# Kernel optimization log

Measured on AMD Instinct MI355X. Metric: run time of the kernel, lower is better.

Reference implementation:

```python
import jax, jax.numpy as jnp
import numpy as np

L, H, E, T, B, V = 8, 16, 1024, 1024, 2, 800
D = E // H  # head_size = 64
STD = 0.02


def setup_inputs() -> dict:
    key = jax.random.key(0)
    ks = iter(jax.random.split(key, 32))

    def nrm(shape):
        return jax.random.normal(next(ks), shape, jnp.float32) * STD

    latlong = jax.random.uniform(next(ks), (B, T, 2), jnp.float32)
    wl = jax.random.uniform(next(ks), (B, T, 1), jnp.float32, minval=3.0, maxval=11.0)
    inp = {
        "idx": jnp.concatenate([latlong, wl], axis=-1),  # [B,T,3]
        "tok_table": nrm((V, E)),
        "pos_W": nrm((2, E)),
        "pos_b": jnp.zeros((E,), jnp.float32),
        # stacked per-layer params (per-head q/k/v linears fused into [E,E])
        "Wq": nrm((L, E, E)),
        "Wk": nrm((L, E, E)),
        "Wv": nrm((L, E, E)),
        "Wo": nrm((L, E, E)),
        "bo": jnp.zeros((L, E), jnp.float32),
        "W1": nrm((L, E, 4 * E)),
        "b1": jnp.zeros((L, 4 * E), jnp.float32),
        "W2": nrm((L, 4 * E, E)),
        "b2": jnp.zeros((L, E), jnp.float32),
        "ln1_g": jnp.ones((L, E), jnp.float32),
        "ln1_b": jnp.zeros((L, E), jnp.float32),
        "ln2_g": jnp.ones((L, E), jnp.float32),
        "ln2_b": jnp.zeros((L, E), jnp.float32),
        "lnf_g": jnp.ones((E,), jnp.float32),
        "lnf_b": jnp.zeros((E,), jnp.float32),
        "lm_W": nrm((E, V)),
        "lm_b": jnp.zeros((V,), jnp.float32),
    }
    return inp


def _ln(x, g, b, eps=1e-5):
    m = x.mean(-1, keepdims=True)
    v = x.var(-1, keepdims=True)
    return (x - m) * jax.lax.rsqrt(v + eps) * g + b


def _block(x, p):
    Wq, Wk, Wv, Wo, bo, W1, b1, W2, b2, g1, be1, g2, be2 = p
    Bx, Tx, _ = x.shape
    h = _ln(x, g1, be1)
    q = (h @ Wq).reshape(Bx, Tx, H, D)
    k = (h @ Wk).reshape(Bx, Tx, H, D)
    v = (h @ Wv).reshape(Bx, Tx, H, D)
    scores = jnp.einsum('bqhd,bkhd->bhqk', q, k) * (D ** -0.5)
    mask = jnp.tril(jnp.ones((Tx, Tx), bool))  # causal
    scores = jnp.where(mask, scores, -jnp.inf)
    w = jax.nn.softmax(scores, axis=-1)  # dropout=0 (eval) -> identity
    attn = jnp.einsum('bhqk,bkhd->bqhd', w, v).reshape(Bx, Tx, E)
    x = x + attn @ Wo + bo
    h = _ln(x, g2, be2)
    x = x + jax.nn.relu(h @ W1 + b1) @ W2 + b2
    return x


def reference(idx, tok_table, pos_W, pos_b, Wq, Wk, Wv, Wo, bo, W1, b1, W2, b2,
              ln1_g, ln1_b, ln2_g, ln2_b, lnf_g, lnf_b, lm_W, lm_b):
    # water level channel -> token id in [0, V-1]
    idx_wl = jnp.clip(jnp.round(idx[..., 2] * 100.0 - 300.0), 0, V - 1).astype(jnp.int32)
    tok_emb = tok_table[idx_wl]                      # [B,T,E]
    pos_emb = idx[..., :2] @ pos_W + pos_b           # [B,T,E]
    x = tok_emb + pos_emb

    params = (Wq, Wk, Wv, Wo, bo, W1, b1, W2, b2, ln1_g, ln1_b, ln2_g, ln2_b)

    def body(carry, p):
        return _block(carry, p), None

    x, _ = jax.lax.scan(body, x, params)
    x = _ln(x, lnf_g, lnf_b)
    logits = x @ lm_W + lm_b                         # [B,T,V]
    return logits
```

## Files before the change

### kernel.cpp

```cpp
#include <hip/hip_runtime.h>
#include <hip/hip_bf16.h>

#define L_ 8
#define H_ 16
#define E_ 1024
#define T_ 1024
#define B_ 2
#define V_ 800
#define D_ 64
#define FF_ 4096
#define N_ (B_ * T_)
#define QS_ 3072

typedef unsigned short u16;
typedef __bf16 bf16x8 __attribute__((ext_vector_type(8)));
typedef float f32x4 __attribute__((ext_vector_type(4)));

__device__ __forceinline__ u16 f2b(float f) {
    unsigned int u = __float_as_uint(f);
    unsigned int r = (u + 0x7fffu + ((u >> 16) & 1u)) >> 16;
    return (u16)r;
}

__device__ __forceinline__ void gld16(const u16* g, u16* l) {
    __builtin_amdgcn_global_load_lds(
        (__attribute__((address_space(1))) void*)(uintptr_t)g,
        (__attribute__((address_space(3))) void*)(unsigned)(uintptr_t)l,
        16, 0, 0);
}

__global__ __launch_bounds__(256) void embed_ln_k(
    const float* __restrict__ idx, const float* __restrict__ tok,
    const float* __restrict__ posW, const float* __restrict__ posb,
    const float* __restrict__ g, const float* __restrict__ bta,
    float* __restrict__ x, u16* __restrict__ out)
{
    __shared__ float rs[4], rq[4];
    int row = blockIdx.x;
    int tid = threadIdx.x;
    int e = tid * 4;
    float lat = idx[row * 3 + 0];
    float lon = idx[row * 3 + 1];
    float wl  = idx[row * 3 + 2];
    float tf = rintf(wl * 100.0f - 300.0f);
    tf = fminf(fmaxf(tf, 0.0f), (float)(V_ - 1));
    int tkn = (int)tf;

    float4 tv = *(const float4*)(tok + (size_t)tkn * E_ + e);
    float4 p0 = *(const float4*)(posW + e);
    float4 p1 = *(const float4*)(posW + E_ + e);
    float4 pb = *(const float4*)(posb + e);
    float4 xv;
    xv.x = tv.x + lat * p0.x + lon * p1.x + pb.x;
    xv.y = tv.y + lat * p0.y + lon * p1.y + pb.y;
    xv.z = tv.z + lat * p0.z + lon * p1.z + pb.z;
    xv.w = tv.w + lat * p0.w + lon * p1.w + pb.w;
    *(float4*)(x + (size_t)row * E_ + e) = xv;

    float s = xv.x + xv.y + xv.z + xv.w;
    float q = xv.x * xv.x + xv.y * xv.y + xv.z * xv.z + xv.w * xv.w;
    #pragma unroll
    for (int off = 32; off; off >>= 1) {
        s += __shfl_xor(s, off, 64);
        q += __shfl_xor(q, off, 64);
    }
    int wv = tid >> 6, ln = tid & 63;
    if (ln == 0) { rs[wv] = s; rq[wv] = q; }
    __syncthreads();
    s = rs[0] + rs[1] + rs[2] + rs[3];
    q = rq[0] + rq[1] + rq[2] + rq[3];
    float mean = s * (1.0f / E_);
    float var  = q * (1.0f / E_) - mean * mean;
    float inv  = 1.0f / sqrtf(var + 1e-5f);
    float4 gv = *(const float4*)(g + e);
    float4 bv = *(const float4*)(bta + e);
    ushort4 ov;
    ov.x = f2b((xv.x - mean) * inv * gv.x + bv.x);
    ov.y = f2b((xv.y - mean) * inv * gv.y + bv.y);
    ov.z = f2b((xv.z - mean) * inv * gv.z + bv.z);
    ov.w = f2b((xv.w - mean) * inv * gv.w + bv.w);
    *(ushort4*)(out + (size_t)row * E_ + e) = ov;
}

__global__ __launch_bounds__(256) void ln_k(
    const float* __restrict__ x, const float* __restrict__ g,
    const float* __restrict__ bta, u16* __restrict__ out)
{
    __shared__ float rs[4], rq[4];
    int row = blockIdx.x;
    int tid = threadIdx.x;
    const float* xr = x + (size_t)row * E_;
    float4 xv = *(const float4*)(xr + tid * 4);
    float s = xv.x + xv.y + xv.z + xv.w;
    float q = xv.x * xv.x + xv.y * xv.y + xv.z * xv.z + xv.w * xv.w;
    #pragma unroll
    for (int off = 32; off; off >>= 1) {
        s += __shfl_xor(s, off, 64);
        q += __shfl_xor(q, off, 64);
    }
    int wv = tid >> 6, ln = tid & 63;
    if (ln == 0) { rs[wv] = s; rq[wv] = q; }
    __syncthreads();
    s = rs[0] + rs[1] + rs[2] + rs[3];
    q = rq[0] + rq[1] + rq[2] + rq[3];
    float mean = s * (1.0f / E_);
    float var  = q * (1.0f / E_) - mean * mean;
    float inv  = 1.0f / sqrtf(var + 1e-5f);
    int c = tid * 4;
    float4 gv = *(const float4*)(g + c);
    float4 bv = *(const float4*)(bta + c);
    ushort4 ov;
    ov.x = f2b((xv.x - mean) * inv * gv.x + bv.x);
    ov.y = f2b((xv.y - mean) * inv * gv.y + bv.y);
    ov.z = f2b((xv.z - mean) * inv * gv.z + bv.z);
    ov.w = f2b((xv.w - mean) * inv * gv.w + bv.w);
    *(ushort4*)(out + (size_t)row * E_ + c) = ov;
}

__device__ __forceinline__ void wtrans_body(
    const float* __restrict__ W, u16* __restrict__ Wt, int K, int M,
    int m0, int k0)
{
    __shared__ float tile[64][65];
    int tid = threadIdx.x;
    int rr = tid >> 4, c4 = (tid & 15) * 4;
    if (m0 + 64 <= M) {
        #pragma unroll
        for (int p = 0; p < 4; p++) {
            int kk = rr + p * 16;
            float4 v4 = *(const float4*)(W + (size_t)(k0 + kk) * M + m0 + c4);
            tile[kk][c4 + 0] = v4.x; tile[kk][c4 + 1] = v4.y;
            tile[kk][c4 + 2] = v4.z; tile[kk][c4 + 3] = v4.w;
        }
    } else {
        #pragma unroll
        for (int p = 0; p < 4; p++) {
            int kk = rr + p * 16;
            const float* wr = W + (size_t)(k0 + kk) * M;
            #pragma unroll
            for (int c = 0; c < 4; c++) {
                int m = m0 + c4 + c;
                tile[kk][c4 + c] = (m < M) ? wr[m] : 0.0f;
            }
        }
    }
    __syncthreads();
    #pragma unroll
    for (int p = 0; p < 4; p++) {
        int ml = rr + p * 16;
        ushort4 o;
        o.x = f2b(tile[c4 + 0][ml]);
        o.y = f2b(tile[c4 + 1][ml]);
        o.z = f2b(tile[c4 + 2][ml]);
        o.w = f2b(tile[c4 + 3][ml]);
        *(ushort4*)(Wt + (size_t)(m0 + ml) * K + k0 + c4) = o;
    }
}

__global__ __launch_bounds__(256) void wtrans_mega_k(
    const float* __restrict__ Wq, const float* __restrict__ Wk,
    const float* __restrict__ Wv, const float* __restrict__ Wo,
    const float* __restrict__ W1, const float* __restrict__ W2,
    const float* __restrict__ lmW,
    u16* __restrict__ wts, u16* __restrict__ wlm_t)
{
    const size_t M1 = 1024 * 1024;
    int bx = blockIdx.x, by = blockIdx.y, z = blockIdx.z;
    if (z == 48) {
        if (bx >= 14) return;
        wtrans_body(lmW, wlm_t, E_, V_, bx * 64, by * 64);
        return;
    }
    int l = z / 6, t = z % 6;
    u16* wb = wts + (size_t)l * 12 * M1;
    size_t oEE = (size_t)l * E_ * E_;
    size_t oEF = (size_t)l * E_ * FF_;
    if (t < 4) {
        if (bx >= 16) return;
        const float* W = (t == 0) ? (Wq + oEE) : (t == 1) ? (Wk + oEE)
                       : (t == 2) ? (Wv + oEE) : (Wo + oEE);
        u16* dst = (t < 3) ? (wb + (size_t)t * M1) : (wb + 3 * M1);
        wtrans_body(W, dst, E_, E_, bx * 64, by * 64);
    } else if (t == 4) {
        wtrans_body(W1 + oEF, wb + 4 * M1, E_, FF_, bx * 64, by * 64);
    } else {
        int id = by * 64 + bx;
        int mb = id >> 6, kb = id & 63;
        wtrans_body(W2 + oEF, wb + 8 * M1, FF_, E_, mb * 64, kb * 64);
    }
}

__global__ __launch_bounds__(256) void gemm_bf16(
    const u16* __restrict__ A, const u16* __restrict__ Bt,
    const float* __restrict__ bias,
    float* __restrict__ Cf, u16* __restrict__ Cb, float* __restrict__ Cp,
    float* __restrict__ Cx, u16* __restrict__ VtOut, int K, int M, int relu)
{
    __shared__ __align__(16) u16 As[3][128 * 32];
    __shared__ __align__(16) u16 Bs[3][128 * 32];
    int tid = threadIdx.x;

    int nx = gridDim.x, ny = gridDim.y;
    int nwg = nx * ny, cpx = nwg >> 3;
    int orig = blockIdx.y * nx + blockIdx.x;
    int wgid = (orig & 7) * cpx + (orig >> 3);
    int bxs = wgid / ny, bys = wgid % ny;
    int bm = bys * 128, bn = bxs * 128;

    int zz = blockIdx.z;
    int kslice = K / (int)gridDim.z;
    int lane = tid & 63, wv = tid >> 6;
    int l15 = lane & 15, q4 = lane >> 4;
    int wm = (wv & 1) * 64, wn = (wv >> 1) * 64;

    const u16* ga = A + (size_t)(bm + (tid >> 2)) * K + zz * kslice + (tid & 3) * 8;
    const u16* gb = Bt + (size_t)(bn + (tid >> 2)) * K + zz * kslice + (tid & 3) * 8;
    size_t gstep = (size_t)64 * K;
    int lofs = wv * (16 * 32);

    f32x4 acc[4][4];
    #pragma unroll
    for (int i = 0; i < 4; i++)
        #pragma unroll
        for (int j = 0; j < 4; j++)
            acc[i][j] = (f32x4){0.0f, 0.0f, 0.0f, 0.0f};

    auto STAGE = [&](int buf, int t) {
        const u16* a0 = ga + t * 32;
        const u16* b0 = gb + t * 32;
        u16* la = &As[buf][0] + lofs;
        u16* lb = &Bs[buf][0] + lofs;
        gld16(a0, la);
        gld16(a0 + gstep, la + 64 * 32);
        gld16(b0, lb);
        gld16(b0 + gstep, lb + 64 * 32);
    };

    int nt = kslice / 32;
    STAGE(0, 0);
    if (nt > 1) STAGE(1, 1);

    for (int t = 0; t < nt; ++t) {
        if (t + 1 < nt)
            asm volatile("s_waitcnt vmcnt(4) lgkmcnt(0)\n\ts_barrier" ::: "memory");
        else
            asm volatile("s_waitcnt vmcnt(0) lgkmcnt(0)\n\ts_barrier" ::: "memory");
        if (t + 2 < nt) STAGE((t + 2) % 3, t + 2);

        int cur = t % 3;
        const bf16x8* Ap = (const bf16x8*)(&As[cur][0]) + (wm + l15) * 4 + q4;
        const bf16x8* Bp = (const bf16x8*)(&Bs[cur][0]) + (wn + l15) * 4 + q4;
        bf16x8 af[4], bg[4];
        #pragma unroll
        for (int i = 0; i < 4; i++) { af[i] = Ap[i * 64]; bg[i] = Bp[i * 64]; }
        __builtin_amdgcn_s_setprio(1);
        #pragma unroll
        for (int i = 0; i < 4; i++)
            #pragma unroll
            for (int j = 0; j < 4; j++)
                acc[i][j] = __builtin_amdgcn_mfma_f32_16x16x32_bf16(
                    af[i], bg[j], acc[i][j], 0, 0, 0);
        __builtin_amdgcn_s_setprio(0);
    }

    size_t poff = (size_t)zz * N_ * M;
    #pragma unroll
    for (int i = 0; i < 4; i++) {
        int r0 = bm + wm + i * 16 + q4 * 4;
        #pragma unroll
        for (int j = 0; j < 4; j++) {
            int col = bn + wn + j * 16 + l15;
            if (col < M) {
                if (Cp) {
                    #pragma unroll
                    for (int r = 0; r < 4; r++)
                        Cp[poff + (size_t)(r0 + r) * M + col] = acc[i][j][r];
                } else if (Cx) {
                    float bv = (bias && zz == 0) ? bias[col] : 0.0f;
                    #pragma unroll
                    for (int r = 0; r < 4; r++)
                        atomicAdd(Cx + (size_t)(r0 + r) * M + col,
                                  acc[i][j][r] + bv);
                } else {
                    float bv = bias ? bias[col] : 0.0f;
                    u16 vb[4];
                    #pragma unroll
                    for (int r = 0; r < 4; r++) {
                        size_t off = (size_t)(r0 + r) * M + col;
                        float v = acc[i][j][r] + bv;
                        if (relu) v = fmaxf(v, 0.0f);
                        u16 hv = f2b(v);
                        vb[r] = hv;
                        if (Cb) Cb[off] = hv; else Cf[off] = v;
                    }
                    if (VtOut && col >= 2 * E_) {
                        int vcol = col - 2 * E_;
                        int hh = vcol >> 6, dd = vcol & 63;
                        int bb = r0 >> 10, t0 = r0 & 1023;
                        *(ushort4*)(VtOut +
                            ((size_t)(bb * H_ + hh) * D_ + dd) * T_ + t0) =
                            *(ushort4*)vb;
                    }
                }
            }
        }
    }
}

__global__ __launch_bounds__(256) void combine_k(
    const float* __restrict__ Cp, const float* __restrict__ bias,
    float* __restrict__ Cf, int M, int total)
{
    int e = (blockIdx.x * 256 + threadIdx.x) * 4;
    if (e >= total) return;
    float4 a = *(const float4*)(Cp + e);
    float4 b = *(const float4*)(Cp + (size_t)total + e);
    a.x += b.x; a.y += b.y; a.z += b.z; a.w += b.w;
    int col = e % M;
    if (bias) {
        float4 bv = *(const float4*)(bias + col);
        a.x += bv.x; a.y += bv.y; a.z += bv.z; a.w += bv.w;
    }
    *(float4*)(Cf + e) = a;
}

__global__ __launch_bounds__(256) void attn_mfma_k(
    const u16* __restrict__ QKV, const u16* __restrict__ Vt,
    u16* __restrict__ O)
{
    __shared__ __align__(16) u16 Ps[4][16 * 72];
    int tid = threadIdx.x;
    int wv = tid >> 6, lane = tid & 63;
    int c = lane & 15, q4 = lane >> 4;
    int qb = (int)(gridDim.x - 1) - (int)blockIdx.x;
    int h = blockIdx.y, b = blockIdx.z;
    int q0 = qb * 64 + wv * 16;
    const float scale = 0.125f;

    const u16* qrow = QKV + (size_t)(b * T_ + q0 + c) * QS_ + h * D_;
    bf16x8 qf0 = *(const bf16x8*)(qrow + q4 * 8);
    bf16x8 qf1 = *(const bf16x8*)(qrow + 32 + q4 * 8);

    const u16* kbase  = QKV + (size_t)b * T_ * QS_ + E_ + h * D_;
    const u16* vtbase = Vt + (size_t)(b * H_ + h) * D_ * T_;

    float l_acc[4] = {0.0f, 0.0f, 0.0f, 0.0f};
    f32x4 acc_o[4];
    #pragma unroll
    for (int nt = 0; nt < 4; nt++) acc_o[nt] = (f32x4){0.f, 0.f, 0.f, 0.f};

    u16* ps = &Ps[wv][0];

    for (int kt = 0; kt <= qb; kt++) {
        int k0 = kt * 64;
        bool diag = (kt == qb);

        bf16x8 kf[4][2];
        #pragma unroll
        for (int j = 0; j < 4; j++) {
            const u16* kr = kbase + (size_t)(k0 + 16 * j + c) * QS_ + q4 * 8;
            kf[j][0] = *(const bf16x8*)(kr);
            kf[j][1] = *(const bf16x8*)(kr + 32);
        }

        #pragma unroll
        for (int j = 0; j < 4; j++) {
            f32x4 sa = (f32x4){0.f, 0.f, 0.f, 0.f};
            sa = __builtin_amdgcn_mfma_f32_16x16x32_bf16(qf0, kf[j][0], sa, 0, 0, 0);
            sa = __builtin_amdgcn_mfma_f32_16x16x32_bf16(qf1, kf[j][1], sa, 0, 0, 0);
            #pragma unroll
            for (int r = 0; r < 4; r++) {
                bool masked = diag && (k0 + 16 * j + c > q0 + 4 * q4 + r);
                float pj = masked ? 0.0f : __expf(sa[r] * scale);
                l_acc[r] += pj;
                ps[(4 * q4 + r) * 72 + 16 * j + c] = f2b(pj);
            }
        }
        bf16x8 pf0 = *(const bf16x8*)(ps + c * 72 + q4 * 8);
        bf16x8 pf1 = *(const bf16x8*)(ps + c * 72 + 32 + q4 * 8);

        bf16x8 vf[4][2];
        #pragma unroll
        for (int nt = 0; nt < 4; nt++) {
            const u16* vr = vtbase + (size_t)(16 * nt + c) * T_ + k0 + q4 * 8;
            vf[nt][0] = *(const bf16x8*)(vr);
            vf[nt][1] = *(const bf16x8*)(vr + 32);
        }

        #pragma unroll
        for (int nt = 0; nt < 4; nt++) {
            acc_o[nt] = __builtin_amdgcn_mfma_f32_16x16x32_bf16(pf0, vf[nt][0], acc_o[nt], 0, 0, 0);
            acc_o[nt] = __builtin_amdgcn_mfma_f32_16x16x32_bf16(pf1, vf[nt][1], acc_o[nt], 0, 0, 0);
        }
    }

    #pragma unroll
    for (int r = 0; r < 4; r++) {
        float ts = l_acc[r];
        ts += __shfl_xor(ts, 1, 64);
        ts += __shfl_xor(ts, 2, 64);
        ts += __shfl_xor(ts, 4, 64);
        ts += __shfl_xor(ts, 8, 64);
        l_acc[r] = ts;
    }

    #pragma unroll
    for (int r = 0; r < 4; r++) {
        float inv = 1.0f / l_acc[r];
        size_t orow = (size_t)(b * T_ + q0 + 4 * q4 + r) * E_ + h * D_;
        #pragma unroll
        for (int nt = 0; nt < 4; nt++)
            O[orow + 16 * nt + c] = f2b(acc_o[nt][r] * inv);
    }
}

extern "C" void kernel_launch(void* const* d_in, const int* in_sizes, int n_in,
                              void* d_out, int out_size, void* d_ws, size_t ws_size,
                              hipStream_t stream)
{
    const float* idx   = (const float*)d_in[0];
    const float* tok   = (const float*)d_in[1];
    const float* posW  = (const float*)d_in[2];
    const float* posb  = (const float*)d_in[3];
    const float* Wq    = (const float*)d_in[4];
    const float* Wk    = (const float*)d_in[5];
    const float* Wv    = (const float*)d_in[6];
    const float* Wo    = (const float*)d_in[7];
    const float* bo    = (const float*)d_in[8];
    const float* W1    = (const float*)d_in[9];
    const float* b1    = (const float*)d_in[10];
    const float* W2    = (const float*)d_in[11];
    const float* b2    = (const float*)d_in[12];
    const float* ln1g  = (const float*)d_in[13];
    const float* ln1b  = (const float*)d_in[14];
    const float* ln2g  = (const float*)d_in[15];
    const float* ln2b  = (const float*)d_in[16];
    const float* lnfg  = (const float*)d_in[17];
    const float* lnfb  = (const float*)d_in[18];
    const float* lmW   = (const float*)d_in[19];
    const float* lmb   = (const float*)d_in[20];
    float* out = (float*)d_out;

    const size_t M1 = 1024 * 1024;
    float* ws    = (float*)d_ws;
    float* x     = ws;
    float* cpart = x + 2 * M1;
    u16* qkv   = (u16*)(cpart + 4 * M1);
    u16* vt    = qkv + 6 * M1;
    u16* h_bf  = vt + 2 * M1;
    u16* ao_bf = h_bf + 2 * M1;
    u16* ff_bf = ao_bf + 2 * M1;
    u16* wts   = ff_bf + 8 * M1;
    u16* wlm_t = wts + 96 * M1;

    dim3 blk(256);
    dim3 gQKV(3072 / 128, N_ / 128, 1);
    dim3 gWo(1024 / 128, N_ / 128, 4);
    dim3 gW1(4096 / 128, N_ / 128, 1);
    dim3 gW2(1024 / 128, N_ / 128, 4);
    dim3 gLM(7, N_ / 128, 2);
    dim3 gAT(T_ / 64, H_, B_);
    dim3 gWT(64, 16, 49);
    int totLM = N_ * V_;
    dim3 cLM(totLM / 4 / 256);

    embed_ln_k<<<N_, blk, 0, stream>>>(idx, tok, posW, posb, ln1g, ln1b,
                                       x, h_bf);
    wtrans_mega_k<<<gWT, blk, 0, stream>>>(Wq, Wk, Wv, Wo, W1, W2, lmW,
                                           wts, wlm_t);

    for (int l = 0; l < L_; l++) {
        size_t oE = (size_t)l * E_;
        size_t oF = (size_t)l * FF_;
        u16* wq_l = wts + (size_t)l * 12 * M1;
        u16* wo_l = wq_l + 3 * M1;
        u16* w1_l = wq_l + 4 * M1;
        u16* w2_l = wq_l + 8 * M1;

        gemm_bf16<<<gQKV, blk, 0, stream>>>(h_bf, wq_l, nullptr,
            nullptr, qkv, nullptr, nullptr, vt, E_, QS_, 0);
        attn_mfma_k<<<gAT, blk, 0, stream>>>(qkv, vt, ao_bf);
        gemm_bf16<<<gWo, blk, 0, stream>>>(ao_bf, wo_l, bo + oE,
            nullptr, nullptr, nullptr, x, nullptr, E_, E_, 0);
        ln_k<<<N_, blk, 0, stream>>>(x, ln2g + oE, ln2b + oE, h_bf);
        gemm_bf16<<<gW1, blk, 0, stream>>>(h_bf, w1_l, b1 + oF,
            nullptr, ff_bf, nullptr, nullptr, nullptr, E_, FF_, 1);
        gemm_bf16<<<gW2, blk, 0, stream>>>(ff_bf, w2_l, b2 + oE,
            nullptr, nullptr, nullptr, x, nullptr, FF_, E_, 0);
        if (l < L_ - 1) {
            ln_k<<<N_, blk, 0, stream>>>(x, ln1g + oE + E_, ln1b + oE + E_, h_bf);
        } else {
            ln_k<<<N_, blk, 0, stream>>>(x, lnfg, lnfb, h_bf);
        }
    }

    gemm_bf16<<<gLM, blk, 0, stream>>>(h_bf, wlm_t, nullptr,
        nullptr, nullptr, cpart, nullptr, nullptr, E_, V_, 0);
    combine_k<<<cLM, blk, 0, stream>>>(cpart, lmb, out, V_, totLM);
}
```

Baseline: 2.115 ms.

## Replace atomic split-K residual adds with partial buffers fused into layernorm

The Wo and W2 split-K GEMMs now write four partial slices to a workspace buffer instead of atomically adding into the residual. A new combined kernel sums the partials, adds bias and residual, writes x back and computes the layernorm in one pass. The attention scale is folded into the Q epilogue of the QKV GEMM, and the weight-transpose grid is flattened to one dimension so no blocks exit idle. This removes float atomics but adds extra partial-buffer traffic and a larger workspace.

```diff
diff --git a/kernel.cpp b/kernel.cpp
--- a/kernel.cpp
+++ b/kernel.cpp
@@ -82,21 +82,35 @@
     *(ushort4*)(out + (size_t)row * E_ + e) = ov;
 }
 
-__global__ __launch_bounds__(256) void ln_k(
-    const float* __restrict__ x, const float* __restrict__ g,
-    const float* __restrict__ bta, u16* __restrict__ out)
+__global__ __launch_bounds__(256) void comb_ln_k(
+    const float* __restrict__ Cp, const float* __restrict__ bias,
+    float* __restrict__ x, const float* __restrict__ g,
+    const float* __restrict__ bta, u16* __restrict__ hout)
 {
     __shared__ float rs[4], rq[4];
     int row = blockIdx.x;
     int tid = threadIdx.x;
-    const float* xr = x + (size_t)row * E_;
-    float4 xv = *(const float4*)(xr + tid * 4);
+    int c = tid * 4;
+    size_t off = (size_t)row * E_ + c;
+    const size_t total = (size_t)N_ * E_;
+    float4 p0 = *(const float4*)(Cp + off);
+    float4 p1 = *(const float4*)(Cp + total + off);
+    float4 p2 = *(const float4*)(Cp + 2 * total + off);
+    float4 p3 = *(const float4*)(Cp + 3 * total + off);
+    float4 xv = *(const float4*)(x + off);
+    float4 bv = *(const float4*)(bias + c);
+    xv.x += p0.x + p1.x + p2.x + p3.x + bv.x;
+    xv.y += p0.y + p1.y + p2.y + p3.y + bv.y;
+    xv.z += p0.z + p1.z + p2.z + p3.z + bv.z;
+    xv.w += p0.w + p1.w + p2.w + p3.w + bv.w;
+    *(float4*)(x + off) = xv;
+
     float s = xv.x + xv.y + xv.z + xv.w;
     float q = xv.x * xv.x + xv.y * xv.y + xv.z * xv.z + xv.w * xv.w;
     #pragma unroll
-    for (int off = 32; off; off >>= 1) {
-        s += __shfl_xor(s, off, 64);
-        q += __shfl_xor(q, off, 64);
+    for (int o = 32; o; o >>= 1) {
+        s += __shfl_xor(s, o, 64);
+        q += __shfl_xor(q, o, 64);
     }
     int wv = tid >> 6, ln = tid & 63;
     if (ln == 0) { rs[wv] = s; rq[wv] = q; }
@@ -106,15 +120,14 @@
     float mean = s * (1.0f / E_);
     float var  = q * (1.0f / E_) - mean * mean;
     float inv  = 1.0f / sqrtf(var + 1e-5f);
-    int c = tid * 4;
     float4 gv = *(const float4*)(g + c);
-    float4 bv = *(const float4*)(bta + c);
+    float4 bb = *(const float4*)(bta + c);
     ushort4 ov;
-    ov.x = f2b((xv.x - mean) * inv * gv.x + bv.x);
-    ov.y = f2b((xv.y - mean) * inv * gv.y + bv.y);
-    ov.z = f2b((xv.z - mean) * inv * gv.z + bv.z);
-    ov.w = f2b((xv.w - mean) * inv * gv.w + bv.w);
-    *(ushort4*)(out + (size_t)row * E_ + c) = ov;
+    ov.x = f2b((xv.x - mean) * inv * gv.x + bb.x);
+    ov.y = f2b((xv.y - mean) * inv * gv.y + bb.y);
+    ov.z = f2b((xv.z - mean) * inv * gv.z + bb.z);
+    ov.w = f2b((xv.w - mean) * inv * gv.w + bb.w);
+    *(ushort4*)(hout + off) = ov;
 }
 
 __device__ __forceinline__ void wtrans_body(
@@ -165,27 +178,31 @@
     u16* __restrict__ wts, u16* __restrict__ wlm_t)
 {
     const size_t M1 = 1024 * 1024;
-    int bx = blockIdx.x, by = blockIdx.y, z = blockIdx.z;
-    if (z == 48) {
-        if (bx >= 14) return;
+    int id = blockIdx.x;
+    if (id >= 24576) {
+        int rr = id - 24576;
+        int bx = rr % 14, by = rr / 14;
         wtrans_body(lmW, wlm_t, E_, V_, bx * 64, by * 64);
         return;
     }
-    int l = z / 6, t = z % 6;
+    int l = id / 3072, r = id % 3072;
     u16* wb = wts + (size_t)l * 12 * M1;
     size_t oEE = (size_t)l * E_ * E_;
     size_t oEF = (size_t)l * E_ * FF_;
-    if (t < 4) {
-        if (bx >= 16) return;
+    if (r < 1024) {
+        int t = r >> 8, rr = r & 255;
+        int bx = rr & 15, by = rr >> 4;
         const float* W = (t == 0) ? (Wq + oEE) : (t == 1) ? (Wk + oEE)
                        : (t == 2) ? (Wv + oEE) : (Wo + oEE);
         u16* dst = (t < 3) ? (wb + (size_t)t * M1) : (wb + 3 * M1);
         wtrans_body(W, dst, E_, E_, bx * 64, by * 64);
-    } else if (t == 4) {
+    } else if (r < 2048) {
+        int rr = r - 1024;
+        int bx = rr & 63, by = rr >> 6;
         wtrans_body(W1 + oEF, wb + 4 * M1, E_, FF_, bx * 64, by * 64);
     } else {
-        int id = by * 64 + bx;
-        int mb = id >> 6, kb = id & 63;
+        int rr = r - 2048;
+        int mb = rr >> 6, kb = rr & 63;
         wtrans_body(W2 + oEF, wb + 8 * M1, FF_, E_, mb * 64, kb * 64);
     }
 }
@@ -194,7 +211,7 @@
     const u16* __restrict__ A, const u16* __restrict__ Bt,
     const float* __restrict__ bias,
     float* __restrict__ Cf, u16* __restrict__ Cb, float* __restrict__ Cp,
-    float* __restrict__ Cx, u16* __restrict__ VtOut, int K, int M, int relu)
+    u16* __restrict__ VtOut, int K, int M, int relu)
 {
     __shared__ __align__(16) u16 As[3][128 * 32];
     __shared__ __align__(16) u16 Bs[3][128 * 32];
@@ -275,19 +292,14 @@
                     #pragma unroll
                     for (int r = 0; r < 4; r++)
                         Cp[poff + (size_t)(r0 + r) * M + col] = acc[i][j][r];
-                } else if (Cx) {
-                    float bv = (bias && zz == 0) ? bias[col] : 0.0f;
-                    #pragma unroll
-                    for (int r = 0; r < 4; r++)
-                        atomicAdd(Cx + (size_t)(r0 + r) * M + col,
-                                  acc[i][j][r] + bv);
                 } else {
                     float bv = bias ? bias[col] : 0.0f;
+                    float sc = (VtOut && col < E_) ? 0.125f : 1.0f;
                     u16 vb[4];
                     #pragma unroll
                     for (int r = 0; r < 4; r++) {
                         size_t off = (size_t)(r0 + r) * M + col;
-                        float v = acc[i][j][r] + bv;
+                        float v = (acc[i][j][r] + bv) * sc;
                         if (relu) v = fmaxf(v, 0.0f);
                         u16 hv = f2b(v);
                         vb[r] = hv;
@@ -335,7 +347,6 @@
     int qb = (int)(gridDim.x - 1) - (int)blockIdx.x;
     int h = blockIdx.y, b = blockIdx.z;
     int q0 = qb * 64 + wv * 16;
-    const float scale = 0.125f;
 
     const u16* qrow = QKV + (size_t)(b * T_ + q0 + c) * QS_ + h * D_;
     bf16x8 qf0 = *(const bf16x8*)(qrow + q4 * 8);
@@ -371,7 +382,7 @@
             #pragma unroll
             for (int r = 0; r < 4; r++) {
                 bool masked = diag && (k0 + 16 * j + c > q0 + 4 * q4 + r);
-                float pj = masked ? 0.0f : __expf(sa[r] * scale);
+                float pj = masked ? 0.0f : __expf(sa[r]);
                 l_acc[r] += pj;
                 ps[(4 * q4 + r) * 72 + 16 * j + c] = f2b(pj);
             }
@@ -445,7 +456,7 @@
     float* ws    = (float*)d_ws;
     float* x     = ws;
     float* cpart = x + 2 * M1;
-    u16* qkv   = (u16*)(cpart + 4 * M1);
+    u16* qkv   = (u16*)(cpart + 8 * M1);
     u16* vt    = qkv + 6 * M1;
     u16* h_bf  = vt + 2 * M1;
     u16* ao_bf = h_bf + 2 * M1;
@@ -460,7 +471,7 @@
     dim3 gW2(1024 / 128, N_ / 128, 4);
     dim3 gLM(7, N_ / 128, 2);
     dim3 gAT(T_ / 64, H_, B_);
-    dim3 gWT(64, 16, 49);
+    dim3 gWT(24800);
     int totLM = N_ * V_;
     dim3 cLM(totLM / 4 / 256);
 
@@ -478,23 +489,26 @@
         u16* w2_l = wq_l + 8 * M1;
 
         gemm_bf16<<<gQKV, blk, 0, stream>>>(h_bf, wq_l, nullptr,
-            nullptr, qkv, nullptr, nullptr, vt, E_, QS_, 0);
+            nullptr, qkv, nullptr, vt, E_, QS_, 0);
         attn_mfma_k<<<gAT, blk, 0, stream>>>(qkv, vt, ao_bf);
-        gemm_bf16<<<gWo, blk, 0, stream>>>(ao_bf, wo_l, bo + oE,
-            nullptr, nullptr, nullptr, x, nullptr, E_, E_, 0);
-        ln_k<<<N_, blk, 0, stream>>>(x, ln2g + oE, ln2b + oE, h_bf);
+        gemm_bf16<<<gWo, blk, 0, stream>>>(ao_bf, wo_l, nullptr,
+            nullptr, nullptr, cpart, nullptr, E_, E_, 0);
+        comb_ln_k<<<N_, blk, 0, stream>>>(cpart, bo + oE, x,
+                                          ln2g + oE, ln2b + oE, h_bf);
         gemm_bf16<<<gW1, blk, 0, stream>>>(h_bf, w1_l, b1 + oF,
-            nullptr, ff_bf, nullptr, nullptr, nullptr, E_, FF_, 1);
-        gemm_bf16<<<gW2, blk, 0, stream>>>(ff_bf, w2_l, b2 + oE,
-            nullptr, nullptr, nullptr, x, nullptr, FF_, E_, 0);
+            nullptr, ff_bf, nullptr, nullptr, E_, FF_, 1);
+        gemm_bf16<<<gW2, blk, 0, stream>>>(ff_bf, w2_l, nullptr,
+            nullptr, nullptr, cpart, nullptr, FF_, E_, 0);
         if (l < L_ - 1) {
-            ln_k<<<N_, blk, 0, stream>>>(x, ln1g + oE + E_, ln1b + oE + E_, h_bf);
+            comb_ln_k<<<N_, blk, 0, stream>>>(cpart, b2 + oE, x,
+                                              ln1g + oE + E_, ln1b + oE + E_, h_bf);
         } else {
-            ln_k<<<N_, blk, 0, stream>>>(x, lnfg, lnfb, h_bf);
+            comb_ln_k<<<N_, blk, 0, stream>>>(cpart, b2 + oE, x,
+                                              lnfg, lnfb, h_bf);
         }
     }
 
     gemm_bf16<<<gLM, blk, 0, stream>>>(h_bf, wlm_t, nullptr,
-        nullptr, nullptr, cpart, nullptr, nullptr, E_, V_, 0);
+        nullptr, nullptr, cpart, nullptr, E_, V_, 0);
     combine_k<<<cLM, blk, 0, stream>>>(cpart, lmb, out, V_, totLM);
 }
```

Measured after the change: 1.962 ms. 7.2% less time.
